# Kernel optimization log

Hardware: AMD Instinct MI355X
Metric: run time of the kernel (lower is better)

Reference implementation:

```python
import jax, jax.numpy as jnp
import numpy as np

CLASS_W = jnp.array([0.3, 3.0, 0.3], dtype=jnp.float32)
GAMMA = 2.0
DICE_SMOOTH = 1.0
SKEL_SMOOTH = 1.0
W_FD, W_SK, W_B = 0.3, 0.3, 0.2
BIG = 1e8  # > max possible squared distance (3*63^2), keeps values finite


def _sq_edt(feature):
    """Exact squared Euclidean distance to nearest True voxel, separable
    per-axis (Felzenszwalb-style lower envelope realized as a brute-force
    min over each line, fully vectorized). feature: bool [B,D,H,W]."""
    d2 = jnp.where(feature, 0.0, BIG).astype(jnp.float32)
    for ax in range(1, d2.ndim):
        L = d2.shape[ax]
        i = jnp.arange(L, dtype=jnp.float32)
        cost = (i[:, None] - i[None, :]) ** 2  # [L, L]
        m = jnp.moveaxis(d2, ax, -1)           # [..., L]
        m = jnp.min(m[..., None, :] + cost, axis=-1)
        d2 = jnp.moveaxis(m, -1, ax)
    return d2


def setup_inputs() -> dict:
    key = jax.random.key(0)
    k1, k2, k3 = jax.random.split(key, 3)
    logits = jax.random.normal(k1, (4, 3, 64, 64, 64), dtype=jnp.float32)
    targets = jax.random.randint(k2, (4, 64, 64, 64), 0, 3, dtype=jnp.int64)
    skeleton = jax.random.randint(k3, (4, 64, 64, 64), 0, 2, dtype=jnp.int32)
    return {"logits": logits, "targets": targets, "skeleton": skeleton}


def reference(logits, targets, skeleton):
    num_classes = logits.shape[1]
    log_p = jax.nn.log_softmax(logits, axis=1)
    probs = jnp.exp(log_p)

    # ---- focal loss ----
    tgt = targets[:, None]  # [B,1,D,H,W]
    p_t = jnp.take_along_axis(probs, tgt, axis=1)[:, 0]
    log_p_t = jnp.take_along_axis(log_p, tgt, axis=1)[:, 0]
    alpha_t = CLASS_W[targets]
    focal = -(alpha_t * (1.0 - p_t) ** GAMMA * log_p_t).mean()

    # ---- dice loss (weighted, per class) ----
    dice = 0.0
    for c in range(num_classes):
        p = probs[:, c]
        t = (targets == c).astype(jnp.float32)
        inter = (p * t).sum()
        union = p.sum() + t.sum()
        dice = dice + CLASS_W[c] * (1.0 - (2.0 * inter + DICE_SMOOTH) / (union + DICE_SMOOTH))
    lfd = focal + dice / CLASS_W.sum()

    # ---- skeleton recall ----
    pred = probs[:, 1]  # surface class
    skel = skeleton.astype(jnp.float32)
    lsk = 1.0 - ((pred * skel).sum() + SKEL_SMOOTH) / (skel.sum() + SKEL_SMOOTH)

    # ---- boundary (signed distance transform) loss ----
    gt = targets == 1
    dt_pos = jnp.sqrt(_sq_edt(gt))    # dist to nearest gt==1
    dt_neg = jnp.sqrt(_sq_edt(~gt))   # dist to nearest gt==0
    signed = dt_pos - dt_neg
    B = gt.shape[0]
    nvox = gt[0].size
    gsum = gt.reshape(B, -1).sum(axis=1)
    mean_pred = pred.mean(axis=(1, 2, 3))
    term = (pred * signed).mean(axis=(1, 2, 3))
    per_b = jnp.where(gsum == 0, mean_pred,
                      jnp.where(gsum == nvox, 1.0 - mean_pred, term))
    lb = per_b.mean()

    total = W_FD * lfd + W_SK * lsk + W_B * lb
    return total, lfd, lsk, lb
```

## Files before the change

kernel.cpp:

```cpp
#include <hip/hip_runtime.h>
#include <math.h>

#define VOXB 262144
#define NVOX 1048576
#define NACC 14
#define PITCH 65
#define NBLK 512

__device__ __forceinline__ float n2side(unsigned long long m, int i) {
    unsigned long long right = m >> i;
    unsigned long long left  = m << (63 - i);
    int dr = right ? __builtin_ctzll(right) : 1000;
    int dl = left  ? __builtin_clzll(left)  : 1000;
    int d  = dr < dl ? dr : dl;
    return (float)(d * d);
}

__global__ __launch_bounds__(512) void edt_wh(const int* __restrict__ targets,
                                              unsigned int* __restrict__ d2wh) {
    __shared__ unsigned int T[64 * PITCH];
    int plane = blockIdx.x >> 1;
    int half  = blockIdx.x & 1;
    int pb    = plane * 4096;
    int wv    = threadIdx.x >> 6;
    int lane  = threadIdx.x & 63;

#pragma unroll
    for (int rt = 0; rt < 8; ++rt) {
        int h = wv * 8 + rt;
        int tv = targets[pb + h * 64 + lane];
        unsigned long long m = __ballot(tv == 1);
        unsigned int p = (unsigned int)fminf(n2side(m, lane), 65535.f);
        unsigned int n = (unsigned int)fminf(n2side(~m, lane), 65535.f);
        T[lane * PITCH + h] = p | (n << 16);
    }
    __syncthreads();

    int hbase = half * 32 + wv * 4;
    float mp[4], mn[4];
#pragma unroll
    for (int rt = 0; rt < 4; ++rt) {
        unsigned int v = T[lane * PITCH + hbase + rt];
        mp[rt] = (float)(v & 0xffffu);
        mn[rt] = (float)(v >> 16);
    }
    for (int r = 1; r < 64; ++r) {
        float rr = (float)(r * r);
        unsigned int vl[4], vr[4];
#pragma unroll
        for (int rt = 0; rt < 4; ++rt) {
            int h = hbase + rt;
            int jl = h - r; jl = jl < 0 ? 0 : jl;
            int jr = h + r; jr = jr > 63 ? 63 : jr;
            vl[rt] = T[lane * PITCH + jl];
            vr[rt] = T[lane * PITCH + jr];
        }
        bool ok = true;
        float thr = (float)((r + 1) * (r + 1));
#pragma unroll
        for (int rt = 0; rt < 4; ++rt) {
            mp[rt] = fminf(mp[rt], fminf((float)(vl[rt] & 0xffffu), (float)(vr[rt] & 0xffffu)) + rr);
            mn[rt] = fminf(mn[rt], fminf((float)(vl[rt] >> 16), (float)(vr[rt] >> 16)) + rr);
            ok = ok && (mp[rt] <= thr) && (mn[rt] <= thr);
        }
        if (__all(ok)) break;
    }
#pragma unroll
    for (int rt = 0; rt < 4; ++rt) {
        unsigned int p = (unsigned int)fminf(mp[rt], 65535.0f);
        unsigned int n = (unsigned int)fminf(mn[rt], 65535.0f);
        d2wh[pb + (hbase + rt) * 64 + lane] = p | (n << 16);
    }
}

__device__ __forceinline__ void vox_accum(float l0, float l1, float l2,
                                          int t, int s, float sd, float* acc) {
    float m  = fmaxf(l0, fmaxf(l1, l2));
    float e0 = __expf(l0 - m), e1 = __expf(l1 - m), e2 = __expf(l2 - m);
    float sum = e0 + e1 + e2;
    float inv = 1.0f / sum;
    float p0 = e0 * inv, p1 = e1 * inv, p2 = e2 * inv;
    float logs = __logf(sum);
    float pt, lpt, alpha;
    if (t == 0)      { pt = p0; lpt = l0 - m - logs; alpha = 0.3f; }
    else if (t == 1) { pt = p1; lpt = l1 - m - logs; alpha = 3.0f; }
    else             { pt = p2; lpt = l2 - m - logs; alpha = 0.3f; }
    float om = 1.0f - pt;
    acc[0] += alpha * om * om * lpt;
    acc[1] += (t == 0) ? p0 : 0.f;
    acc[2] += (t == 1) ? p1 : 0.f;
    acc[3] += (t == 2) ? p2 : 0.f;
    acc[4] += p0; acc[5] += p1; acc[6] += p2;
    acc[7] += (t == 0) ? 1.f : 0.f;
    acc[8] += (t == 1) ? 1.f : 0.f;
    acc[9] += (t == 2) ? 1.f : 0.f;
    float fs = (float)s;
    acc[10] += p1 * fs;
    acc[11] += fs;
    acc[12] += p1;
    acc[13] += p1 * sd;
}

__global__ __launch_bounds__(512) void edt_d_reduce(
        const float* __restrict__ logits, const int* __restrict__ targets,
        const int* __restrict__ skel, const unsigned int* __restrict__ d2wh,
        float* __restrict__ partials) {
    __shared__ unsigned int T[64 * PITCH];
    __shared__ float red[8][NACC];
    int slab = blockIdx.x >> 1;
    int half = blockIdx.x & 1;
    int b = slab >> 6, h = slab & 63;
    int vb = b * VOXB + h * 64;
    int t = threadIdx.x;

#pragma unroll
    for (int k = 0; k < 2; ++k) {
        int f  = k * 512 + t;
        int d  = f >> 4;
        int w0 = (f & 15) * 4;
        uint4 q = *reinterpret_cast<const uint4*>(d2wh + vb + d * 4096 + w0);
        T[(w0 + 0) * PITCH + d] = q.x;
        T[(w0 + 1) * PITCH + d] = q.y;
        T[(w0 + 2) * PITCH + d] = q.z;
        T[(w0 + 3) * PITCH + d] = q.w;
    }
    __syncthreads();

    int wv = t >> 6, lane = t & 63;
    int dbase = half * 32 + wv * 4;

    int   tv[4], sv[4];
    float l0[4], l1[4], l2[4];
#pragma unroll
    for (int rt = 0; rt < 4; ++rt) {
        int d = dbase + rt;
        int voff = vb + d * 4096 + lane;
        tv[rt] = targets[voff];
        sv[rt] = skel[voff];
        size_t lb = (size_t)b * (3 * VOXB) + d * 4096 + h * 64 + lane;
        l0[rt] = logits[lb];
        l1[rt] = logits[lb + VOXB];
        l2[rt] = logits[lb + 2 * VOXB];
    }

    float mp[4], mn[4];
#pragma unroll
    for (int rt = 0; rt < 4; ++rt) {
        unsigned int v = T[lane * PITCH + dbase + rt];
        mp[rt] = (float)(v & 0xffffu);
        mn[rt] = (float)(v >> 16);
    }
    for (int r = 1; r < 64; ++r) {
        float rr = (float)(r * r);
        unsigned int vl[4], vr[4];
#pragma unroll
        for (int rt = 0; rt < 4; ++rt) {
            int d = dbase + rt;
            int jl = d - r; jl = jl < 0 ? 0 : jl;
            int jr = d + r; jr = jr > 63 ? 63 : jr;
            vl[rt] = T[lane * PITCH + jl];
            vr[rt] = T[lane * PITCH + jr];
        }
        bool ok = true;
        float thr = (float)((r + 1) * (r + 1));
#pragma unroll
        for (int rt = 0; rt < 4; ++rt) {
            mp[rt] = fminf(mp[rt], fminf((float)(vl[rt] & 0xffffu), (float)(vr[rt] & 0xffffu)) + rr);
            mn[rt] = fminf(mn[rt], fminf((float)(vl[rt] >> 16), (float)(vr[rt] >> 16)) + rr);
            ok = ok && (mp[rt] <= thr) && (mn[rt] <= thr);
        }
        if (__all(ok)) break;
    }

    float acc[NACC];
#pragma unroll
    for (int k = 0; k < NACC; ++k) acc[k] = 0.f;
#pragma unroll
    for (int rt = 0; rt < 4; ++rt) {
        float sd = sqrtf(mp[rt]) - sqrtf(mn[rt]);
        vox_accum(l0[rt], l1[rt], l2[rt], tv[rt], sv[rt], sd, acc);
    }

#pragma unroll
    for (int k = 0; k < NACC; ++k) {
        float v = acc[k];
#pragma unroll
        for (int off = 32; off; off >>= 1) v += __shfl_down(v, off, 64);
        if (lane == 0) red[wv][k] = v;
    }
    __syncthreads();
    if (t < NACC) {
        float v = 0.f;
#pragma unroll
        for (int q = 0; q < 8; ++q) v += red[q][t];
        partials[t * NBLK + blockIdx.x] = v;
    }
}

__global__ __launch_bounds__(256) void final_reduce(
        const float* __restrict__ partials, float* __restrict__ out) {
    __shared__ float sb[NACC][4];
    int w = threadIdx.x >> 6, lane = threadIdx.x & 63;
#pragma unroll
    for (int k = 0; k < NACC; ++k) {
        const float* p = partials + k * NBLK + w * 128;
        float v = p[lane] + p[lane + 64];
#pragma unroll
        for (int off = 32; off; off >>= 1) v += __shfl_down(v, off, 64);
        if (lane == 0) sb[k][w] = v;
    }
    __syncthreads();
    if (threadIdx.x == 0) {
        double S[NACC];
#pragma unroll
        for (int k = 0; k < NACC; ++k)
            S[k] = (double)sb[k][0] + sb[k][1] + sb[k][2] + sb[k][3];
        const double W[3] = {0.3, 3.0, 0.3};
        double focal = -S[0] / (double)NVOX;
        double dice = 0.0;
        for (int c = 0; c < 3; ++c)
            dice += W[c] * (1.0 - (2.0 * S[1 + c] + 1.0) /
                                  (S[4 + c] + S[7 + c] + 1.0));
        double lfd = focal + dice / 3.6;
        double lsk = 1.0 - (S[10] + 1.0) / (S[11] + 1.0);
        double lb = 0.0;
        for (int bb = 0; bb < 4; ++bb) {
            double gs = sb[8][bb];
            double ps = sb[12][bb];
            double tm = sb[13][bb];
            double per;
            if (gs == 0.0)               per = ps / (double)VOXB;
            else if (gs == (double)VOXB) per = 1.0 - ps / (double)VOXB;
            else                         per = tm / (double)VOXB;
            lb += per;
        }
        lb *= 0.25;
        double total = 0.3 * lfd + 0.3 * lsk + 0.2 * lb;
        out[0] = (float)total;
        out[1] = (float)lfd;
        out[2] = (float)lsk;
        out[3] = (float)lb;
    }
}

extern "C" void kernel_launch(void* const* d_in, const int* in_sizes, int n_in,
                              void* d_out, int out_size, void* d_ws, size_t ws_size,
                              hipStream_t stream) {
    const float* logits  = (const float*)d_in[0];
    const int*   targets = (const int*)d_in[1];
    const int*   skel    = (const int*)d_in[2];
    unsigned int* d2wh   = (unsigned int*)d_ws;
    float* partials      = (float*)(d2wh + NVOX);
    float* out = (float*)d_out;

    edt_wh<<<NBLK, 512, 0, stream>>>(targets, d2wh);
    edt_d_reduce<<<NBLK, 512, 0, stream>>>(logits, targets, skel, d2wh,
                                           partials);
    final_reduce<<<1, 256, 0, stream>>>(partials, out);
}
```

Baseline: 29.71 us.

## Reorder EDT passes and pack target/skeleton bits into distance words

The first kernel now does the W and D passes on H-slabs and packs the target class and skeleton bit into the top four bits of each 32-bit distance word, narrowing each distance field to 14 bits. The second kernel runs the H pass on D-planes and reads target and skeleton from the packed word, so it no longer loads those two int arrays. This removes global traffic from the second kernel and lets the logits loads overlap the shared-memory transpose before the barrier. In exchange the first kernel does strided slab reads of targets and skel, and distances are clamped at 16383, which is still above the largest possible squared distance here.

```diff
diff --git a/kernel.cpp b/kernel.cpp
--- a/kernel.cpp
+++ b/kernel.cpp
@@ -6,6 +6,7 @@
 #define NACC 14
 #define PITCH 65
 #define NBLK 512
+#define D2CLAMP 16383.0f
 
 __device__ __forceinline__ float n2side(unsigned long long m, int i) {
     unsigned long long right = m >> i;
@@ -16,42 +17,49 @@
     return (float)(d * d);
 }
 
-__global__ __launch_bounds__(512) void edt_wh(const int* __restrict__ targets,
-                                              unsigned int* __restrict__ d2wh) {
+__global__ __launch_bounds__(512) void edt_wd(const int* __restrict__ targets,
+                                              const int* __restrict__ skel,
+                                              unsigned int* __restrict__ d2) {
     __shared__ unsigned int T[64 * PITCH];
-    int plane = blockIdx.x >> 1;
-    int half  = blockIdx.x & 1;
-    int pb    = plane * 4096;
-    int wv    = threadIdx.x >> 6;
-    int lane  = threadIdx.x & 63;
+    int slab = blockIdx.x >> 1;
+    int half = blockIdx.x & 1;
+    int b = slab >> 6, h = slab & 63;
+    int base = b * VOXB + h * 64;
+    int wv   = threadIdx.x >> 6;
+    int lane = threadIdx.x & 63;
 
 #pragma unroll
     for (int rt = 0; rt < 8; ++rt) {
-        int h = wv * 8 + rt;
-        int tv = targets[pb + h * 64 + lane];
+        int d = wv * 8 + rt;
+        int off = base + d * 4096 + lane;
+        int tv = targets[off];
+        int sv = skel[off];
         unsigned long long m = __ballot(tv == 1);
-        unsigned int p = (unsigned int)fminf(n2side(m, lane), 65535.f);
-        unsigned int n = (unsigned int)fminf(n2side(~m, lane), 65535.f);
-        T[lane * PITCH + h] = p | (n << 16);
-    }
-    __syncthreads();
-
-    int hbase = half * 32 + wv * 4;
+        unsigned int p = (unsigned int)fminf(n2side(m, lane), D2CLAMP);
+        unsigned int n = (unsigned int)fminf(n2side(~m, lane), D2CLAMP);
+        T[lane * PITCH + d] = p | (n << 14) | ((unsigned int)tv << 28)
+                                | ((unsigned int)sv << 30);
+    }
+    __syncthreads();
+
+    int dbase = half * 32 + wv * 4;
     float mp[4], mn[4];
-#pragma unroll
-    for (int rt = 0; rt < 4; ++rt) {
-        unsigned int v = T[lane * PITCH + hbase + rt];
-        mp[rt] = (float)(v & 0xffffu);
-        mn[rt] = (float)(v >> 16);
+    unsigned int ts[4];
+#pragma unroll
+    for (int rt = 0; rt < 4; ++rt) {
+        unsigned int v = T[lane * PITCH + dbase + rt];
+        mp[rt] = (float)(v & 16383u);
+        mn[rt] = (float)((v >> 14) & 16383u);
+        ts[rt] = v >> 28;
     }
     for (int r = 1; r < 64; ++r) {
         float rr = (float)(r * r);
         unsigned int vl[4], vr[4];
 #pragma unroll
         for (int rt = 0; rt < 4; ++rt) {
-            int h = hbase + rt;
-            int jl = h - r; jl = jl < 0 ? 0 : jl;
-            int jr = h + r; jr = jr > 63 ? 63 : jr;
+            int d = dbase + rt;
+            int jl = d - r; jl = jl < 0 ? 0 : jl;
+            int jr = d + r; jr = jr > 63 ? 63 : jr;
             vl[rt] = T[lane * PITCH + jl];
             vr[rt] = T[lane * PITCH + jr];
         }
@@ -59,17 +67,19 @@
         float thr = (float)((r + 1) * (r + 1));
 #pragma unroll
         for (int rt = 0; rt < 4; ++rt) {
-            mp[rt] = fminf(mp[rt], fminf((float)(vl[rt] & 0xffffu), (float)(vr[rt] & 0xffffu)) + rr);
-            mn[rt] = fminf(mn[rt], fminf((float)(vl[rt] >> 16), (float)(vr[rt] >> 16)) + rr);
+            mp[rt] = fminf(mp[rt], fminf((float)(vl[rt] & 16383u),
+                                         (float)(vr[rt] & 16383u)) + rr);
+            mn[rt] = fminf(mn[rt], fminf((float)((vl[rt] >> 14) & 16383u),
+                                         (float)((vr[rt] >> 14) & 16383u)) + rr);
             ok = ok && (mp[rt] <= thr) && (mn[rt] <= thr);
         }
         if (__all(ok)) break;
     }
 #pragma unroll
     for (int rt = 0; rt < 4; ++rt) {
-        unsigned int p = (unsigned int)fminf(mp[rt], 65535.0f);
-        unsigned int n = (unsigned int)fminf(mn[rt], 65535.0f);
-        d2wh[pb + (hbase + rt) * 64 + lane] = p | (n << 16);
+        unsigned int p = (unsigned int)fminf(mp[rt], D2CLAMP);
+        unsigned int n = (unsigned int)fminf(mn[rt], D2CLAMP);
+        d2[base + (dbase + rt) * 4096 + lane] = p | (n << 14) | (ts[rt] << 28);
     }
 }
 
@@ -101,63 +111,59 @@
     acc[13] += p1 * sd;
 }
 
-__global__ __launch_bounds__(512) void edt_d_reduce(
-        const float* __restrict__ logits, const int* __restrict__ targets,
-        const int* __restrict__ skel, const unsigned int* __restrict__ d2wh,
+__global__ __launch_bounds__(512) void edt_h_reduce(
+        const float* __restrict__ logits, const unsigned int* __restrict__ d2,
         float* __restrict__ partials) {
     __shared__ unsigned int T[64 * PITCH];
     __shared__ float red[8][NACC];
-    int slab = blockIdx.x >> 1;
-    int half = blockIdx.x & 1;
-    int b = slab >> 6, h = slab & 63;
-    int vb = b * VOXB + h * 64;
+    int plane = blockIdx.x >> 1;
+    int half  = blockIdx.x & 1;
+    int b = plane >> 6, d = plane & 63;
+    int pbase = b * VOXB + d * 4096;
     int t = threadIdx.x;
+    int wv = t >> 6, lane = t & 63;
+    int hbase = half * 32 + wv * 4;
 
 #pragma unroll
     for (int k = 0; k < 2; ++k) {
         int f  = k * 512 + t;
-        int d  = f >> 4;
+        int h  = f >> 4;
         int w0 = (f & 15) * 4;
-        uint4 q = *reinterpret_cast<const uint4*>(d2wh + vb + d * 4096 + w0);
-        T[(w0 + 0) * PITCH + d] = q.x;
-        T[(w0 + 1) * PITCH + d] = q.y;
-        T[(w0 + 2) * PITCH + d] = q.z;
-        T[(w0 + 3) * PITCH + d] = q.w;
-    }
-    __syncthreads();
-
-    int wv = t >> 6, lane = t & 63;
-    int dbase = half * 32 + wv * 4;
-
-    int   tv[4], sv[4];
+        uint4 q = *reinterpret_cast<const uint4*>(d2 + pbase + h * 64 + w0);
+        T[(w0 + 0) * PITCH + h] = q.x;
+        T[(w0 + 1) * PITCH + h] = q.y;
+        T[(w0 + 2) * PITCH + h] = q.z;
+        T[(w0 + 3) * PITCH + h] = q.w;
+    }
+
     float l0[4], l1[4], l2[4];
-#pragma unroll
-    for (int rt = 0; rt < 4; ++rt) {
-        int d = dbase + rt;
-        int voff = vb + d * 4096 + lane;
-        tv[rt] = targets[voff];
-        sv[rt] = skel[voff];
-        size_t lb = (size_t)b * (3 * VOXB) + d * 4096 + h * 64 + lane;
+    size_t lbase = (size_t)b * (3 * VOXB) + d * 4096;
+#pragma unroll
+    for (int rt = 0; rt < 4; ++rt) {
+        size_t lb = lbase + (hbase + rt) * 64 + lane;
         l0[rt] = logits[lb];
         l1[rt] = logits[lb + VOXB];
         l2[rt] = logits[lb + 2 * VOXB];
     }
+    __syncthreads();
 
     float mp[4], mn[4];
-#pragma unroll
-    for (int rt = 0; rt < 4; ++rt) {
-        unsigned int v = T[lane * PITCH + dbase + rt];
-        mp[rt] = (float)(v & 0xffffu);
-        mn[rt] = (float)(v >> 16);
+    unsigned int ts[4];
+#pragma unroll
+    for (int rt = 0; rt < 4; ++rt) {
+        unsigned int v = T[lane * PITCH + hbase + rt];
+        mp[rt] = (float)(v & 16383u);
+        mn[rt] = (float)((v >> 14) & 16383u);
+        ts[rt] = v >> 28;
     }
     for (int r = 1; r < 64; ++r) {
         float rr = (float)(r * r);
         unsigned int vl[4], vr[4];
 #pragma unroll
         for (int rt = 0; rt < 4; ++rt) {
-            int d = dbase + rt;
-            int jl = d - r; jl = jl < 0 ? 0 : jl;
-            int jr = d + r; jr = jr > 63 ? 63 : jr;
+            int h = hbase + rt;
+            int jl = h - r; jl = jl < 0 ? 0 : jl;
+            int jr = h + r; jr = jr > 63 ? 63 : jr;
             vl[rt] = T[lane * PITCH + jl];
             vr[rt] = T[lane * PITCH + jr];
         }
@@ -165,8 +171,10 @@
         float thr = (float)((r + 1) * (r + 1));
 #pragma unroll
         for (int rt = 0; rt < 4; ++rt) {
-            mp[rt] = fminf(mp[rt], fminf((float)(vl[rt] & 0xffffu), (float)(vr[rt] & 0xffffu)) + rr);
-            mn[rt] = fminf(mn[rt], fminf((float)(vl[rt] >> 16), (float)(vr[rt] >> 16)) + rr);
+            mp[rt] = fminf(mp[rt], fminf((float)(vl[rt] & 16383u),
+                                         (float)(vr[rt] & 16383u)) + rr);
+            mn[rt] = fminf(mn[rt], fminf((float)((vl[rt] >> 14) & 16383u),
+                                         (float)((vr[rt] >> 14) & 16383u)) + rr);
             ok = ok && (mp[rt] <= thr) && (mn[rt] <= thr);
         }
         if (__all(ok)) break;
@@ -178,7 +186,8 @@
 #pragma unroll
     for (int rt = 0; rt < 4; ++rt) {
         float sd = sqrtf(mp[rt]) - sqrtf(mn[rt]);
-        vox_accum(l0[rt], l1[rt], l2[rt], tv[rt], sv[rt], sd, acc);
+        vox_accum(l0[rt], l1[rt], l2[rt], (int)(ts[rt] & 3u),
+                  (int)(ts[rt] >> 2), sd, acc);
     }
 
 #pragma unroll
@@ -249,12 +258,11 @@
     const float* logits  = (const float*)d_in[0];
     const int*   targets = (const int*)d_in[1];
     const int*   skel    = (const int*)d_in[2];
-    unsigned int* d2wh   = (unsigned int*)d_ws;
-    float* partials      = (float*)(d2wh + NVOX);
+    unsigned int* d2     = (unsigned int*)d_ws;
+    float* partials      = (float*)(d2 + NVOX);
     float* out = (float*)d_out;
 
-    edt_wh<<<NBLK, 512, 0, stream>>>(targets, d2wh);
-    edt_d_reduce<<<NBLK, 512, 0, stream>>>(logits, targets, skel, d2wh,
-                                           partials);
+    edt_wd<<<NBLK, 512, 0, stream>>>(targets, skel, d2);
+    edt_h_reduce<<<NBLK, 512, 0, stream>>>(logits, d2, partials);
     final_reduce<<<1, 256, 0, stream>>>(partials, out);
 }
```

Measured after the change: 30.88 us. 3.9% more time.

## Replace W/H EDT intermediate with per-line D bitmasks and fuse EDT into reduce

Applied to the files above, without the earlier changes.

The first kernel now packs the targets==1 indicator along the D axis into 64-bit masks per (b,h,w) line, a 128KB intermediate instead of a 4MB d2 buffer. The reduce kernel loads the batch's masks into shared memory and computes the D-axis distance with bit scans. It then runs the W and H passes in shared memory per plane and accumulates the loss terms directly. This removes the large global write and read of the intermediate, but each block recomputes the full-plane W pass even though it handles only half the plane, which duplicates work and raises shared memory use.

```diff
diff --git a/kernel.cpp b/kernel.cpp
--- a/kernel.cpp
+++ b/kernel.cpp
@@ -16,60 +16,27 @@
     return (float)(d * d);
 }
 
-__global__ __launch_bounds__(512) void edt_wh(const int* __restrict__ targets,
-                                              unsigned int* __restrict__ d2wh) {
-    __shared__ unsigned int T[64 * PITCH];
-    int plane = blockIdx.x >> 1;
-    int half  = blockIdx.x & 1;
-    int pb    = plane * 4096;
-    int wv    = threadIdx.x >> 6;
-    int lane  = threadIdx.x & 63;
-
+__global__ __launch_bounds__(512) void build_masks(
+        const int* __restrict__ targets, unsigned long long* __restrict__ Mask) {
+    __shared__ unsigned long long Mp[8][64];
+    int slab = blockIdx.x;
+    int b = slab >> 6, h = slab & 63;
+    int wv = threadIdx.x >> 6, lane = threadIdx.x & 63;
+    int base = b * VOXB + h * 64 + lane;
+    unsigned long long bits = 0;
 #pragma unroll
     for (int rt = 0; rt < 8; ++rt) {
-        int h = wv * 8 + rt;
-        int tv = targets[pb + h * 64 + lane];
-        unsigned long long m = __ballot(tv == 1);
-        unsigned int p = (unsigned int)fminf(n2side(m, lane), 65535.f);
-        unsigned int n = (unsigned int)fminf(n2side(~m, lane), 65535.f);
-        T[lane * PITCH + h] = p | (n << 16);
-    }
-    __syncthreads();
-
-    int hbase = half * 32 + wv * 4;
-    float mp[4], mn[4];
-#pragma unroll
-    for (int rt = 0; rt < 4; ++rt) {
-        unsigned int v = T[lane * PITCH + hbase + rt];
-        mp[rt] = (float)(v & 0xffffu);
-        mn[rt] = (float)(v >> 16);
-    }
-    for (int r = 1; r < 64; ++r) {
-        float rr = (float)(r * r);
-        unsigned int vl[4], vr[4];
-#pragma unroll
-        for (int rt = 0; rt < 4; ++rt) {
-            int h = hbase + rt;
-            int jl = h - r; jl = jl < 0 ? 0 : jl;
-            int jr = h + r; jr = jr > 63 ? 63 : jr;
-            vl[rt] = T[lane * PITCH + jl];
-            vr[rt] = T[lane * PITCH + jr];
-        }
-        bool ok = true;
-        float thr = (float)((r + 1) * (r + 1));
-#pragma unroll
-        for (int rt = 0; rt < 4; ++rt) {
-            mp[rt] = fminf(mp[rt], fminf((float)(vl[rt] & 0xffffu), (float)(vr[rt] & 0xffffu)) + rr);
-            mn[rt] = fminf(mn[rt], fminf((float)(vl[rt] >> 16), (float)(vr[rt] >> 16)) + rr);
-            ok = ok && (mp[rt] <= thr) && (mn[rt] <= thr);
-        }
-        if (__all(ok)) break;
-    }
-#pragma unroll
-    for (int rt = 0; rt < 4; ++rt) {
-        unsigned int p = (unsigned int)fminf(mp[rt], 65535.0f);
-        unsigned int n = (unsigned int)fminf(mn[rt], 65535.0f);
-        d2wh[pb + (hbase + rt) * 64 + lane] = p | (n << 16);
+        int d = wv * 8 + rt;
+        int tv = targets[base + d * 4096];
+        bits |= ((unsigned long long)(tv == 1)) << d;
+    }
+    Mp[wv][lane] = bits;
+    __syncthreads();
+    if (wv == 0) {
+        unsigned long long m = Mp[0][lane] | Mp[1][lane] | Mp[2][lane] |
+                               Mp[3][lane] | Mp[4][lane] | Mp[5][lane] |
+                               Mp[6][lane] | Mp[7][lane];
+        Mask[slab * 64 + lane] = m;
     }
 }
 
@@ -101,84 +68,129 @@
     acc[13] += p1 * sd;
 }
 
-__global__ __launch_bounds__(512) void edt_d_reduce(
+__global__ __launch_bounds__(512) void edt_reduce(
         const float* __restrict__ logits, const int* __restrict__ targets,
-        const int* __restrict__ skel, const unsigned int* __restrict__ d2wh,
+        const int* __restrict__ skel, const unsigned long long* __restrict__ Mask,
         float* __restrict__ partials) {
+    __shared__ unsigned long long Msk[4096];
+    __shared__ unsigned int V0[64 * 64];
     __shared__ unsigned int T[64 * PITCH];
     __shared__ float red[8][NACC];
-    int slab = blockIdx.x >> 1;
-    int half = blockIdx.x & 1;
-    int b = slab >> 6, h = slab & 63;
-    int vb = b * VOXB + h * 64;
+    int plane = blockIdx.x >> 1;
+    int half  = blockIdx.x & 1;
+    int b = plane >> 6, d0 = plane & 63;
     int t = threadIdx.x;
-
-#pragma unroll
-    for (int k = 0; k < 2; ++k) {
-        int f  = k * 512 + t;
-        int d  = f >> 4;
-        int w0 = (f & 15) * 4;
-        uint4 q = *reinterpret_cast<const uint4*>(d2wh + vb + d * 4096 + w0);
-        T[(w0 + 0) * PITCH + d] = q.x;
-        T[(w0 + 1) * PITCH + d] = q.y;
-        T[(w0 + 2) * PITCH + d] = q.z;
-        T[(w0 + 3) * PITCH + d] = q.w;
-    }
-    __syncthreads();
-
     int wv = t >> 6, lane = t & 63;
-    int dbase = half * 32 + wv * 4;
-
+    int hbase = half * 32 + wv * 4;
+
+    int pbase = b * VOXB + d0 * 4096;
     int   tv[4], sv[4];
     float l0[4], l1[4], l2[4];
+    size_t lbase = (size_t)b * (3 * VOXB) + d0 * 4096;
 #pragma unroll
     for (int rt = 0; rt < 4; ++rt) {
-        int d = dbase + rt;
-        int voff = vb + d * 4096 + lane;
-        tv[rt] = targets[voff];
-        sv[rt] = skel[voff];
-        size_t lb = (size_t)b * (3 * VOXB) + d * 4096 + h * 64 + lane;
+        int off = pbase + (hbase + rt) * 64 + lane;
+        tv[rt] = targets[off];
+        sv[rt] = skel[off];
+        size_t lb = lbase + (hbase + rt) * 64 + lane;
         l0[rt] = logits[lb];
         l1[rt] = logits[lb + VOXB];
         l2[rt] = logits[lb + 2 * VOXB];
     }
 
-    float mp[4], mn[4];
-#pragma unroll
-    for (int rt = 0; rt < 4; ++rt) {
-        unsigned int v = T[lane * PITCH + dbase + rt];
-        mp[rt] = (float)(v & 0xffffu);
-        mn[rt] = (float)(v >> 16);
-    }
-    for (int r = 1; r < 64; ++r) {
-        float rr = (float)(r * r);
-        unsigned int vl[4], vr[4];
+#pragma unroll
+    for (int k = 0; k < 8; ++k)
+        Msk[k * 512 + t] = Mask[b * 4096 + k * 512 + t];
+    __syncthreads();
+
+#pragma unroll
+    for (int rt = 0; rt < 8; ++rt) {
+        int h = wv * 8 + rt;
+        unsigned long long m = Msk[h * 64 + lane];
+        unsigned int p = (unsigned int)fminf(n2side(m, d0), 65535.f);
+        unsigned int n = (unsigned int)fminf(n2side(~m, d0), 65535.f);
+        V0[h * 64 + lane] = p | (n << 16);
+    }
+    __syncthreads();
+
+    {
+        float mp[8], mn[8];
+#pragma unroll
+        for (int rt = 0; rt < 8; ++rt) {
+            unsigned int v = V0[(wv * 8 + rt) * 64 + lane];
+            mp[rt] = (float)(v & 0xffffu);
+            mn[rt] = (float)(v >> 16);
+        }
+        for (int r = 1; r < 64; ++r) {
+            float rr = (float)(r * r);
+            int jl = lane - r; jl = jl < 0 ? 0 : jl;
+            int jr = lane + r; jr = jr > 63 ? 63 : jr;
+            unsigned int vl[8], vr[8];
+#pragma unroll
+            for (int rt = 0; rt < 8; ++rt) {
+                vl[rt] = V0[(wv * 8 + rt) * 64 + jl];
+                vr[rt] = V0[(wv * 8 + rt) * 64 + jr];
+            }
+            bool ok = true;
+            float thr = (float)((r + 1) * (r + 1));
+#pragma unroll
+            for (int rt = 0; rt < 8; ++rt) {
+                mp[rt] = fminf(mp[rt], fminf((float)(vl[rt] & 0xffffu),
+                                             (float)(vr[rt] & 0xffffu)) + rr);
+                mn[rt] = fminf(mn[rt], fminf((float)(vl[rt] >> 16),
+                                             (float)(vr[rt] >> 16)) + rr);
+                ok = ok && (mp[rt] <= thr) && (mn[rt] <= thr);
+            }
+            if (__all(ok)) break;
+        }
+#pragma unroll
+        for (int rt = 0; rt < 8; ++rt) {
+            unsigned int p = (unsigned int)fminf(mp[rt], 65535.f);
+            unsigned int n = (unsigned int)fminf(mn[rt], 65535.f);
+            T[lane * PITCH + wv * 8 + rt] = p | (n << 16);
+        }
+    }
+    __syncthreads();
+
+    float acc[NACC];
+#pragma unroll
+    for (int k = 0; k < NACC; ++k) acc[k] = 0.f;
+    {
+        float mp[4], mn[4];
 #pragma unroll
         for (int rt = 0; rt < 4; ++rt) {
-            int d = dbase + rt;
-            int jl = d - r; jl = jl < 0 ? 0 : jl;
-            int jr = d + r; jr = jr > 63 ? 63 : jr;
-            vl[rt] = T[lane * PITCH + jl];
-            vr[rt] = T[lane * PITCH + jr];
-        }
-        bool ok = true;
-        float thr = (float)((r + 1) * (r + 1));
+            unsigned int v = T[lane * PITCH + hbase + rt];
+            mp[rt] = (float)(v & 0xffffu);
+            mn[rt] = (float)(v >> 16);
+        }
+        for (int r = 1; r < 64; ++r) {
+            float rr = (float)(r * r);
+            unsigned int vl[4], vr[4];
+#pragma unroll
+            for (int rt = 0; rt < 4; ++rt) {
+                int h = hbase + rt;
+                int jl = h - r; jl = jl < 0 ? 0 : jl;
+                int jr = h + r; jr = jr > 63 ? 63 : jr;
+                vl[rt] = T[lane * PITCH + jl];
+                vr[rt] = T[lane * PITCH + jr];
+            }
+            bool ok = true;
+            float thr = (float)((r + 1) * (r + 1));
+#pragma unroll
+            for (int rt = 0; rt < 4; ++rt) {
+                mp[rt] = fminf(mp[rt], fminf((float)(vl[rt] & 0xffffu),
+                                             (float)(vr[rt] & 0xffffu)) + rr);
+                mn[rt] = fminf(mn[rt], fminf((float)(vl[rt] >> 16),
+                                             (float)(vr[rt] >> 16)) + rr);
+                ok = ok && (mp[rt] <= thr) && (mn[rt] <= thr);
+            }
+            if (__all(ok)) break;
+        }
 #pragma unroll
         for (int rt = 0; rt < 4; ++rt) {
-            mp[rt] = fminf(mp[rt], fminf((float)(vl[rt] & 0xffffu), (float)(vr[rt] & 0xffffu)) + rr);
-            mn[rt] = fminf(mn[rt], fminf((float)(vl[rt] >> 16), (float)(vr[rt] >> 16)) + rr);
-            ok = ok && (mp[rt] <= thr) && (mn[rt] <= thr);
-        }
-        if (__all(ok)) break;
-    }
-
-    float acc[NACC];
-#pragma unroll
-    for (int k = 0; k < NACC; ++k) acc[k] = 0.f;
-#pragma unroll
-    for (int rt = 0; rt < 4; ++rt) {
-        float sd = sqrtf(mp[rt]) - sqrtf(mn[rt]);
-        vox_accum(l0[rt], l1[rt], l2[rt], tv[rt], sv[rt], sd, acc);
+            float sd = sqrtf(mp[rt]) - sqrtf(mn[rt]);
+            vox_accum(l0[rt], l1[rt], l2[rt], tv[rt], sv[rt], sd, acc);
+        }
     }
 
 #pragma unroll
@@ -249,12 +261,11 @@
     const float* logits  = (const float*)d_in[0];
     const int*   targets = (const int*)d_in[1];
     const int*   skel    = (const int*)d_in[2];
-    unsigned int* d2wh   = (unsigned int*)d_ws;
-    float* partials      = (float*)(d2wh + NVOX);
+    unsigned long long* Mask = (unsigned long long*)d_ws;
+    float* partials = (float*)(Mask + 16384);
     float* out = (float*)d_out;
 
-    edt_wh<<<NBLK, 512, 0, stream>>>(targets, d2wh);
-    edt_d_reduce<<<NBLK, 512, 0, stream>>>(logits, targets, skel, d2wh,
-                                           partials);
+    build_masks<<<256, 512, 0, stream>>>(targets, Mask);
+    edt_reduce<<<NBLK, 512, 0, stream>>>(logits, targets, skel, Mask, partials);
     final_reduce<<<1, 256, 0, stream>>>(partials, out);
 }
```

Result: slower. 32.49 us (+9.3%).
